# Optimization experiments

Hardware: AMD Instinct MI355X
Metric: run time of the kernel (lower is better)

## Reference

```python
import jax, jax.numpy as jnp
import numpy as np

N, H, F, E, K = 4096, 512, 2048, 8, 2  # tokens, hidden, ffn(=4H), experts, top_k


def setup_inputs() -> dict:
    key = jax.random.key(0)
    ks = jax.random.split(key, 7)
    def w(k, shape, fan_in):
        return jax.random.normal(k, shape, dtype=jnp.float32) * (fan_in ** -0.5)
    return {
        "x": jax.random.normal(ks[0], (N, H), dtype=jnp.float32),
        "W_in": w(ks[1], (H, H), H),          # input_proj.weight  [out,in]
        "W_router": w(ks[2], (E, H), H),      # router.gate.weight [E,H]
        "W_gate": w(ks[3], (E, F, H), H),     # per-expert gate_proj.weight
        "W_up": w(ks[4], (E, F, H), H),       # per-expert up_proj.weight
        "W_down": w(ks[5], (E, H, F), F),     # per-expert down_proj.weight
        "W_out": w(ks[6], (H, H), H),         # output_proj.weight
    }


def reference(x, W_in, W_router, W_gate, W_up, W_down, W_out):
    h = x @ W_in.T                                  # [N,H] input_proj
    logits = h @ W_router.T                         # [N,E]
    # route_mode='balanced' and world_size==1 -> expert_bias is None
    probs = jax.nn.softmax(logits, axis=-1)
    top_w, top_i = jax.lax.top_k(probs, K)          # [N,K]
    top_w = jax.nn.softmax(top_w, axis=-1)          # renormalize over top-k

    # per-token combine weight for each expert: [N,E]
    onehot = jax.nn.one_hot(top_i, E, dtype=h.dtype)      # [N,K,E]
    combine_w = jnp.einsum('nk,nke->ne', top_w, onehot)

    def expert(wg, wu, wd):
        # SwiGLU FFN: down( silu(gate(h)) * up(h) )
        return (jax.nn.silu(h @ wg.T) * (h @ wu.T)) @ wd.T  # [N,H]

    expert_out = jax.vmap(expert)(W_gate, W_up, W_down)     # [E,N,H]
    combined = jnp.einsum('ne,enh->nh', combine_w, expert_out)
    return combined @ W_out.T                                # output_proj
```

## Files before the change

kernel.cpp:

```cpp
#include <hip/hip_runtime.h>
#include <hip/hip_bf16.h>

typedef unsigned short u16;
typedef unsigned int u32;
typedef short bf16x8 __attribute__((ext_vector_type(8)));
typedef float f32x4 __attribute__((ext_vector_type(4)));

#define AS1 __attribute__((address_space(1)))
#define AS3 __attribute__((address_space(3)))

#define NTOK 4096
#define HDIM 512
#define FDIM 2048
#define NEXP 8
#define NASSIGN (NTOK * 2)
#define NPAD2 (NASSIGN + NEXP * 256)
#define RBMAX 128

__device__ __forceinline__ void g2l16(const void* g, void* l) {
  __builtin_amdgcn_global_load_lds((const AS1 u32*)g, (AS3 u32*)l, 16, 0, 0);
}
__device__ __forceinline__ u16 f2bf(float f) {
  u32 u = __float_as_uint(f);
  u = (u + 0x7FFFu + ((u >> 16) & 1u)) >> 16;
  return (u16)u;
}
__device__ __forceinline__ float bf2f(u16 h) { return __uint_as_float(((u32)h) << 16); }
__device__ __forceinline__ u32 pkbf(float a, float b) {
  __hip_bfloat162 h = __float22bfloat162_rn(float2{a, b});
  u32 r;
  __builtin_memcpy(&r, &h, 4);
  return r;
}
__device__ __forceinline__ int4 pk8(const float4 a, const float4 b) {
  int4 r;
  r.x = (int)pkbf(a.x, a.y); r.y = (int)pkbf(a.z, a.w);
  r.z = (int)pkbf(b.x, b.y); r.w = (int)pkbf(b.z, b.w);
  return r;
}

#define WAITV4() asm volatile("s_waitcnt vmcnt(4)" ::: "memory")
#define WAITV0() asm volatile("s_waitcnt vmcnt(0)" ::: "memory")
#define LGKM0() asm volatile("s_waitcnt lgkmcnt(0)" ::: "memory")
#define BAR() __builtin_amdgcn_s_barrier()
#define SCB() __builtin_amdgcn_sched_barrier(0)
#define PRIO1() __builtin_amdgcn_s_setprio(1)
#define PRIO0() __builtin_amdgcn_s_setprio(0)
#define VMBAR() do { WAITV0(); BAR(); } while (0)

__global__ __launch_bounds__(256) void cvtall_kernel(
    const float* __restrict__ x, const float* __restrict__ Wi, const float* __restrict__ Wo,
    const float* __restrict__ Wg, const float* __restrict__ Wu, const float* __restrict__ Wd,
    u16* __restrict__ xb, u16* __restrict__ Wib, u16* __restrict__ Wob,
    u16* __restrict__ Wgb, u16* __restrict__ Wub, u16* __restrict__ Wdb) {
  const int c = blockIdx.x, tid = threadIdx.x;
  const float* s; u16* d; int cs;
  if (c < 128) { s = x; d = xb; cs = 0; }
  else if (c < 144) { s = Wi; d = Wib; cs = 128; }
  else if (c < 160) { s = Wo; d = Wob; cs = 144; }
  else if (c < 672) { s = Wg; d = Wgb; cs = 160; }
  else if (c < 1184) { s = Wu; d = Wub; cs = 672; }
  else { s = Wd; d = Wdb; cs = 1184; }
  const size_t base = (size_t)(c - cs) * 16384 + (size_t)tid * 8;
  const float* sp = s + base;
  u16* dp = d + base;
  float4 a[16];
#pragma unroll
  for (int j = 0; j < 8; ++j) {
    a[2 * j] = *(const float4*)(sp + j * 2048);
    a[2 * j + 1] = *(const float4*)(sp + j * 2048 + 4);
  }
#pragma unroll
  for (int j = 0; j < 8; ++j)
    *(int4*)(dp + j * 2048) = pk8(a[2 * j], a[2 * j + 1]);
}

__global__ __launch_bounds__(256) void wreff_kernel(
    const float* __restrict__ Wr, const float* __restrict__ Wi, double* __restrict__ wre) {
  const int t = blockIdx.x * 256 + threadIdx.x;
  const int e = t >> 9, k = t & 511;
  const float* wr = Wr + e * HDIM;
  double a0 = 0.0, a1 = 0.0, a2 = 0.0, a3 = 0.0;
  for (int j = 0; j < HDIM; j += 4) {
    a0 += (double)wr[j + 0] * (double)Wi[(j + 0) * HDIM + k];
    a1 += (double)wr[j + 1] * (double)Wi[(j + 1) * HDIM + k];
    a2 += (double)wr[j + 2] * (double)Wi[(j + 2) * HDIM + k];
    a3 += (double)wr[j + 3] * (double)Wi[(j + 3) * HDIM + k];
  }
  wre[t] = (a0 + a1) + (a2 + a3);
}

__global__ __launch_bounds__(128) void router_kernel(
    const float* __restrict__ x, const double* __restrict__ wre,
    int* __restrict__ idx, float* __restrict__ wts) {
  __shared__ double lw[NEXP * HDIM];
  for (int i = threadIdx.x; i < NEXP * HDIM; i += 128) lw[i] = wre[i];
  __syncthreads();
  const int n = blockIdx.x * 128 + threadIdx.x;
  const float* xr = x + (size_t)n * HDIM;
  double acc[NEXP] = {};
  for (int k4 = 0; k4 < HDIM / 4; ++k4) {
    const float4 xv = ((const float4*)xr)[k4];
    const float xc[4] = {xv.x, xv.y, xv.z, xv.w};
#pragma unroll
    for (int c = 0; c < 4; ++c) {
      const double xd = (double)xc[c];
#pragma unroll
      for (int e = 0; e < NEXP; ++e) acc[e] += xd * lw[e * HDIM + k4 * 4 + c];
    }
  }
  double mx = acc[0];
#pragma unroll
  for (int e = 1; e < NEXP; ++e) mx = acc[e] > mx ? acc[e] : mx;
  double p[NEXP], se = 0.0;
#pragma unroll
  for (int e = 0; e < NEXP; ++e) { p[e] = exp(acc[e] - mx); se += p[e]; }
  const double inv = 1.0 / se;
#pragma unroll
  for (int e = 0; e < NEXP; ++e) p[e] *= inv;
  int i0 = 0; double b0 = p[0];
#pragma unroll
  for (int e = 1; e < NEXP; ++e) if (p[e] > b0) { b0 = p[e]; i0 = e; }
  int i1 = -1; double b1 = -1.0;
#pragma unroll
  for (int e = 0; e < NEXP; ++e) if (e != i0 && p[e] > b1) { b1 = p[e]; i1 = e; }
  const double e0 = exp(b0), e1 = exp(b1);
  idx[2 * n] = i0; idx[2 * n + 1] = i1;
  wts[2 * n] = (float)(e0 / (e0 + e1));
  wts[2 * n + 1] = (float)(e1 / (e0 + e1));
}

__global__ void assign_kernel(const int* __restrict__ idx, int* __restrict__ tok,
                              int* __restrict__ pos, int* __restrict__ rbe2,
                              int* __restrict__ rbp2, int* __restrict__ rbe1,
                              int* __restrict__ rbp1, int* __restrict__ nrb) {
  __shared__ int cnt[NEXP], cur[NEXP];
  const int tid = threadIdx.x;
  if (tid < NEXP) cnt[tid] = 0;
  __syncthreads();
  for (int a = tid; a < NASSIGN; a += 256) atomicAdd(&cnt[idx[a]], 1);
  __syncthreads();
  if (tid == 0) {
    int o = 0, n2 = 0, n1 = 0;
    for (int e = 0; e < NEXP; ++e) {
      cur[e] = o;
      const int nb2 = (cnt[e] + 255) >> 8;
      const int nb1 = (cnt[e] + 127) >> 7;
      for (int i = 0; i < nb2; ++i) { rbe2[n2] = e; rbp2[n2] = o + i * 256; ++n2; }
      for (int i = 0; i < nb1; ++i) { rbe1[n1] = e; rbp1[n1] = o + i * 128; ++n1; }
      o += nb2 * 256;
    }
    nrb[0] = n2; nrb[1] = n1;
  }
  __syncthreads();
  for (int p = tid; p < NPAD2; p += 256) tok[p] = 0;
  __syncthreads();
  for (int a = tid; a < NASSIGN; a += 256) {
    const int e = idx[a];
    const int q = atomicAdd(&cur[e], 1);
    tok[q] = a >> 1;
    pos[a] = q;
  }
}

template <int SB, int NT>
__device__ __forceinline__ void gemm128_body(
    const u16* __restrict__ A, const u16* __restrict__ B, void* __restrict__ C,
    int m0, int n0, int N, int K, u16* sm, int tid) {
  u16 *lA0 = sm, *lA1 = sm + 8192, *lB0 = sm + 16384, *lB1 = sm + 24576;
  const int w = tid >> 6, l = tid & 63;
  const int wm = (w >> 2) * 64, wn = (w & 3) * 32;
  const int lm = l & 15, lk = (l >> 4) * 8, xr = (l & 7) << 3;
  const int sr = l >> 3, sc = ((l & 7) ^ sr) * 8;
  const u16* As = A + (size_t)(m0 + w * 8 + sr) * K + sc;
  const u16* Bs = B + (size_t)(n0 + w * 8 + sr) * K + sc;
  f32x4 acc[4][2] = {};
  auto STG = [&](u16* dA, u16* dB, int kt) {
    g2l16(As + kt, dA + w * 512);
    g2l16(As + (size_t)64 * K + kt, dA + 4096 + w * 512);
    g2l16(Bs + kt, dB + w * 512);
    g2l16(Bs + (size_t)64 * K + kt, dB + 4096 + w * 512);
  };
  auto CMP = [&](const u16* a_, const u16* b_) {
#pragma unroll
    for (int kk = 0; kk < 2; ++kk) {
      const int ko = (kk * 32 + lk) ^ xr;
      bf16x8 af[4], bf[2];
#pragma unroll
      for (int i = 0; i < 4; ++i) af[i] = *(const bf16x8*)(a_ + (wm + i * 16 + lm) * 64 + ko);
#pragma unroll
      for (int j = 0; j < 2; ++j) bf[j] = *(const bf16x8*)(b_ + (wn + j * 16 + lm) * 64 + ko);
      PRIO1();
#pragma unroll
      for (int i = 0; i < 4; ++i)
#pragma unroll
        for (int j = 0; j < 2; ++j)
          acc[i][j] = __builtin_amdgcn_mfma_f32_16x16x32_bf16(af[i], bf[j], acc[i][j], 0, 0, 0);
      PRIO0();
    }
  };
  STG(lA0, lB0, 0);
  VMBAR();
  for (int t = 0; t < NT; t += 2) {
    if (t + 1 < NT) STG(lA1, lB1, (t + 1) * 64);
    CMP(lA0, lB0);
    VMBAR();
    if (t + 2 < NT) STG(lA0, lB0, (t + 2) * 64);
    CMP(lA1, lB1);
    VMBAR();
  }
  const int cr = (l >> 4) * 4, cc = lm;
#pragma unroll
  for (int i = 0; i < 4; ++i)
#pragma unroll
    for (int j = 0; j < 2; ++j)
#pragma unroll
      for (int r = 0; r < 4; ++r) {
        const size_t o = (size_t)(m0 + wm + i * 16 + cr + r) * N + n0 + wn + j * 16 + cc;
        if (SB) ((u16*)C)[o] = f2bf(acc[i][j][r]);
        else ((float*)C)[o] = acc[i][j][r];
      }
}

__global__ __launch_bounds__(512, 2) void ingemm_kernel(
    const u16* __restrict__ xb, const u16* __restrict__ Wib, u16* __restrict__ hb) {
  __shared__ __align__(16) u16 sm[32768];
  gemm128_body<1, 8>(xb, Wib, hb, blockIdx.y * 128, blockIdx.x * 128, HDIM, HDIM, sm, threadIdx.x);
}

__global__ __launch_bounds__(512, 2) void outgemm_kernel(
    const u16* __restrict__ cb, const u16* __restrict__ Wob, float* __restrict__ out) {
  __shared__ __align__(16) u16 sm[32768];
  gemm128_body<0, 8>(cb, Wob, out, blockIdx.y * 128, blockIdx.x * 128, HDIM, HDIM, sm, threadIdx.x);
}

__global__ __launch_bounds__(512, 2) void gateup_kernel(
    const u16* __restrict__ hb, const u16* __restrict__ Wg, const u16* __restrict__ Wu,
    u16* __restrict__ act, const int* __restrict__ tok, const int* __restrict__ rbe2,
    const int* __restrict__ rbp2, const int* __restrict__ nrb) {
  const int rb = blockIdx.y;
  if (rb >= nrb[0]) return;
  __shared__ __align__(16) u16 sm[65536];
  const int e = rbe2[rb], p0 = rbp2[rb], n0 = blockIdx.x * 128;
  const int tid = threadIdx.x, w = tid >> 6, l = tid & 63;
  const int half = w >> 2, rh = (w >> 1) & 1, ch = w & 1;
  const int lm = l & 15, lk = (l >> 4) * 8, xr = (l & 7) << 3;
  const int sr = l >> 3, sc = ((l & 7) ^ sr) * 8;
  const u16* Asrc[4];
#pragma unroll
  for (int c = 0; c < 4; ++c)
    Asrc[c] = hb + (size_t)tok[p0 + c * 64 + w * 8 + sr] * HDIM + sc;
  const u16 *Gsrc[2], *Usrc[2];
#pragma unroll
  for (int c = 0; c < 2; ++c) {
    Gsrc[c] = Wg + (size_t)e * FDIM * HDIM + (size_t)(n0 + c * 64 + w * 8 + sr) * HDIM + sc;
    Usrc[c] = Wu + (size_t)e * FDIM * HDIM + (size_t)(n0 + c * 64 + w * 8 + sr) * HDIM + sc;
  }
  f32x4 acc[8][4] = {};
  auto STG = [&](int b, int kt) {
    u16* d = sm + b * 32768;
#pragma unroll
    for (int c = 0; c < 4; ++c) g2l16(Asrc[c] + kt, d + c * 4096 + w * 512);
#pragma unroll
    for (int c = 0; c < 2; ++c) {
      g2l16(Gsrc[c] + kt, d + 16384 + c * 4096 + w * 512);
      g2l16(Usrc[c] + kt, d + 24576 + c * 4096 + w * 512);
    }
  };
  auto CMP = [&](int b) {
    const u16* A_ = sm + b * 32768;
    const u16* B_ = A_ + 16384 + half * 8192;
#pragma unroll
    for (int kk = 0; kk < 2; ++kk) {
      const int ko = (kk * 32 + lk) ^ xr;
      bf16x8 af[8], bf[4];
#pragma unroll
      for (int i = 0; i < 8; ++i)
        af[i] = *(const bf16x8*)(A_ + (rh * 128 + i * 16 + lm) * 64 + ko);
#pragma unroll
      for (int j = 0; j < 4; ++j)
        bf[j] = *(const bf16x8*)(B_ + (ch * 64 + j * 16 + lm) * 64 + ko);
      PRIO1();
#pragma unroll
      for (int i = 0; i < 8; ++i)
#pragma unroll
        for (int j = 0; j < 4; ++j)
          acc[i][j] = __builtin_amdgcn_mfma_f32_16x16x32_bf16(af[i], bf[j], acc[i][j], 0, 0, 0);
      PRIO0();
    }
  };
  STG(0, 0);
  VMBAR();
#pragma unroll
  for (int t = 0; t < 8; ++t) {
    if (t < 7) STG((t + 1) & 1, (t + 1) * 64);
    CMP(t & 1);
    VMBAR();
  }
  const int cr = (l >> 4) * 4, cc = lm;
  float* red = (float*)sm;
  if (half == 1) {
#pragma unroll
    for (int i = 0; i < 8; ++i)
#pragma unroll
      for (int j = 0; j < 4; ++j)
        *(f32x4*)&red[(w - 4) * 8192 + (i * 4 + j) * 256 + l * 4] = acc[i][j];
  }
  LGKM0();
  BAR();
  if (half == 0) {
#pragma unroll
    for (int i = 0; i < 8; ++i)
#pragma unroll
      for (int j = 0; j < 4; ++j) {
        const f32x4 ua = *(const f32x4*)&red[w * 8192 + (i * 4 + j) * 256 + l * 4];
#pragma unroll
        for (int r = 0; r < 4; ++r) {
          const float g = acc[i][j][r], u = ua[r];
          const float s = g / (1.0f + __expf(-g));
          act[(size_t)(p0 + rh * 128 + i * 16 + cr + r) * FDIM + n0 + ch * 64 + j * 16 + cc] =
              f2bf(s * u);
        }
      }
  }
}

__global__ __launch_bounds__(512, 2) void down_kernel(
    const u16* __restrict__ act, const u16* __restrict__ Wd, u16* __restrict__ dwn,
    const int* __restrict__ rbe1, const int* __restrict__ rbp1, const int* __restrict__ nrb) {
  const int rb = blockIdx.y;
  if (rb >= nrb[1]) return;
  __shared__ __align__(16) u16 sm[49152];
  const int e = rbe1[rb], p0 = rbp1[rb], n0 = blockIdx.x * 128;
  const int tid = threadIdx.x, w = tid >> 6, l = tid & 63;
  const int g = w >> 2;
  const int wm = ((w >> 1) & 1) * 64, wn = (w & 1) * 64;
  const int lm = l & 15, lk = (l >> 4) * 8, xr = (l & 7) << 3;
  const int ko = (g * 32 + lk) ^ xr;
  const int sr = l >> 3, sc = ((l & 7) ^ sr) * 8;
  const u16* As = act + (size_t)(p0 + w * 8 + sr) * FDIM + sc;
  const u16* Bs = Wd + (size_t)e * HDIM * FDIM + (size_t)(n0 + w * 8 + sr) * FDIM + sc;
  f32x4 acc[4][4] = {};
  auto STG = [&](int b, int kt) {
    u16* d = sm + b * 16384;
    g2l16(As + kt, d + w * 512);
    g2l16(As + (size_t)64 * FDIM + kt, d + 4096 + w * 512);
    g2l16(Bs + kt, d + 8192 + w * 512);
    g2l16(Bs + (size_t)64 * FDIM + kt, d + 12288 + w * 512);
  };
  auto CMP = [&](int b) {
    const u16* a_ = sm + b * 16384;
    const u16* b_ = a_ + 8192;
    bf16x8 af[4], bf[4];
#pragma unroll
    for (int i = 0; i < 4; ++i) af[i] = *(const bf16x8*)(a_ + (wm + i * 16 + lm) * 64 + ko);
#pragma unroll
    for (int j = 0; j < 4; ++j) bf[j] = *(const bf16x8*)(b_ + (wn + j * 16 + lm) * 64 + ko);
#pragma unroll
    for (int i = 0; i < 4; ++i)
#pragma unroll
      for (int j = 0; j < 4; ++j)
        acc[i][j] = __builtin_amdgcn_mfma_f32_16x16x32_bf16(af[i], bf[j], acc[i][j], 0, 0, 0);
  };
  STG(0, 0); STG(1, 64);
  WAITV4(); BAR();
#pragma unroll
  for (int t = 0; t < 32; ++t) {
    if (t + 2 < 32) STG((t + 2) % 3, (t + 2) * 64);
    CMP(t % 3);
    if (t + 2 < 32) WAITV4(); else WAITV0();
    BAR();
  }
  LGKM0();
  SCB();
  BAR();
  float* red = (float*)sm;
  if (g == 1) {
#pragma unroll
    for (int i = 0; i < 4; ++i)
#pragma unroll
      for (int j = 0; j < 4; ++j)
        *(f32x4*)&red[(w & 3) * 4096 + (i * 4 + j) * 256 + l * 4] = acc[i][j];
  }
  BAR();
  if (g == 0) {
    const int cr = (l >> 4) * 4, cc = lm;
#pragma unroll
    for (int i = 0; i < 4; ++i)
#pragma unroll
      for (int j = 0; j < 4; ++j) {
        const f32x4 o = *(const f32x4*)&red[w * 4096 + (i * 4 + j) * 256 + l * 4];
        const f32x4 s = acc[i][j] + o;
#pragma unroll
        for (int r = 0; r < 4; ++r)
          dwn[(size_t)(p0 + wm + i * 16 + cr + r) * HDIM + n0 + wn + j * 16 + cc] = f2bf(s[r]);
      }
  }
}

__global__ void combine_kernel(const u16* __restrict__ dwn, const int* __restrict__ pos,
                               const float* __restrict__ wts, u16* __restrict__ cb) {
  const int n = blockIdx.x, t = threadIdx.x;
  const int p0 = pos[2 * n], p1 = pos[2 * n + 1];
  const float w0 = wts[2 * n], w1 = wts[2 * n + 1];
  const ushort4 a = ((const ushort4*)(dwn + (size_t)p0 * HDIM))[t];
  const ushort4 b = ((const ushort4*)(dwn + (size_t)p1 * HDIM))[t];
  ushort4 o;
  o.x = f2bf(w0 * bf2f(a.x) + w1 * bf2f(b.x));
  o.y = f2bf(w0 * bf2f(a.y) + w1 * bf2f(b.y));
  o.z = f2bf(w0 * bf2f(a.z) + w1 * bf2f(b.z));
  o.w = f2bf(w0 * bf2f(a.w) + w1 * bf2f(b.w));
  ((ushort4*)(cb + (size_t)n * HDIM))[t] = o;
}

extern "C" void kernel_launch(void* const* d_in, const int* in_sizes, int n_in,
                              void* d_out, int out_size, void* d_ws, size_t ws_size,
                              hipStream_t stream) {
  const float* x  = (const float*)d_in[0];
  const float* Wi = (const float*)d_in[1];
  const float* Wr = (const float*)d_in[2];
  const float* Wg = (const float*)d_in[3];
  const float* Wu = (const float*)d_in[4];
  const float* Wd = (const float*)d_in[5];
  const float* Wo = (const float*)d_in[6];
  float* out = (float*)d_out;

  char* ws = (char*)d_ws;
  size_t off = 0;
  auto alloc = [&](size_t bytes) -> void* {
    off = (off + 255) & ~(size_t)255;
    void* p = ws + off;
    off += bytes;
    return p;
  };
  u16* xb   = (u16*)alloc((size_t)NTOK * HDIM * 2);
  u16* hb   = (u16*)alloc((size_t)NTOK * HDIM * 2);
  u16* cb   = (u16*)alloc((size_t)NTOK * HDIM * 2);
  u16* Wib  = (u16*)alloc((size_t)HDIM * HDIM * 2);
  u16* Wob  = (u16*)alloc((size_t)HDIM * HDIM * 2);
  u16* Wgb  = (u16*)alloc((size_t)NEXP * FDIM * HDIM * 2);
  u16* Wub  = (u16*)alloc((size_t)NEXP * FDIM * HDIM * 2);
  u16* Wdb  = (u16*)alloc((size_t)NEXP * HDIM * FDIM * 2);
  u16* actb = (u16*)alloc((size_t)NPAD2 * FDIM * 2);
  u16* dwn  = (u16*)alloc((size_t)NPAD2 * HDIM * 2);
  double* wre = (double*)alloc((size_t)NEXP * HDIM * 8);
  int* idx = (int*)alloc((size_t)NASSIGN * 4);
  float* wts = (float*)alloc((size_t)NASSIGN * 4);
  int* tok = (int*)alloc((size_t)NPAD2 * 4);
  int* pos = (int*)alloc((size_t)NASSIGN * 4);
  int* rbe2 = (int*)alloc((size_t)RBMAX * 4);
  int* rbp2 = (int*)alloc((size_t)RBMAX * 4);
  int* rbe1 = (int*)alloc((size_t)RBMAX * 4);
  int* rbp1 = (int*)alloc((size_t)RBMAX * 4);
  int* nrb = (int*)alloc(256);

  cvtall_kernel<<<1696, 256, 0, stream>>>(x, Wi, Wo, Wg, Wu, Wd, xb, Wib, Wob, Wgb, Wub, Wdb);
  wreff_kernel<<<16, 256, 0, stream>>>(Wr, Wi, wre);
  router_kernel<<<32, 128, 0, stream>>>(x, wre, idx, wts);
  assign_kernel<<<1, 256, 0, stream>>>(idx, tok, pos, rbe2, rbp2, rbe1, rbp1, nrb);
  ingemm_kernel<<<dim3(4, 32), 512, 0, stream>>>(xb, Wib, hb);
  gateup_kernel<<<dim3(16, 40), 512, 0, stream>>>(hb, Wgb, Wub, actb, tok, rbe2, rbp2, nrb);
  down_kernel<<<dim3(4, 72), 512, 0, stream>>>(actb, Wdb, dwn, rbe1, rbp1, nrb);
  combine_kernel<<<NTOK, 128, 0, stream>>>(dwn, pos, wts, cb);
  outgemm_kernel<<<dim3(4, 32), 512, 0, stream>>>(cb, Wob, out);
}
```

Before: 235.2 us.

## Restructure gate/up GEMM main loop into 4-phase interleaved LDS-load/MFMA schedule

```diff
diff --git a/kernel.cpp b/kernel.cpp
--- a/kernel.cpp
+++ b/kernel.cpp
@@ -243,82 +243,117 @@
   __shared__ __align__(16) u16 sm[65536];
   const int e = rbe2[rb], p0 = rbp2[rb], n0 = blockIdx.x * 128;
   const int tid = threadIdx.x, w = tid >> 6, l = tid & 63;
-  const int half = w >> 2, rh = (w >> 1) & 1, ch = w & 1;
+  const int wr = w >> 2, wc = w & 3;
   const int lm = l & 15, lk = (l >> 4) * 8, xr = (l & 7) << 3;
   const int sr = l >> 3, sc = ((l & 7) ^ sr) * 8;
+  const int ko0 = lk ^ xr, ko1 = (32 + lk) ^ xr;
   const u16* Asrc[4];
 #pragma unroll
   for (int c = 0; c < 4; ++c)
     Asrc[c] = hb + (size_t)tok[p0 + c * 64 + w * 8 + sr] * HDIM + sc;
-  const u16 *Gsrc[2], *Usrc[2];
+  const u16 *Gs[2], *Us[2];
 #pragma unroll
   for (int c = 0; c < 2; ++c) {
-    Gsrc[c] = Wg + (size_t)e * FDIM * HDIM + (size_t)(n0 + c * 64 + w * 8 + sr) * HDIM + sc;
-    Usrc[c] = Wu + (size_t)e * FDIM * HDIM + (size_t)(n0 + c * 64 + w * 8 + sr) * HDIM + sc;
+    Gs[c] = Wg + (size_t)e * FDIM * HDIM + (size_t)(n0 + c * 64 + w * 8 + sr) * HDIM + sc;
+    Us[c] = Wu + (size_t)e * FDIM * HDIM + (size_t)(n0 + c * 64 + w * 8 + sr) * HDIM + sc;
   }
   f32x4 acc[8][4] = {};
-  auto STG = [&](int b, int kt) {
-    u16* d = sm + b * 32768;
-#pragma unroll
-    for (int c = 0; c < 4; ++c) g2l16(Asrc[c] + kt, d + c * 4096 + w * 512);
+  auto STGA = [&](int b, int kt) {
+#pragma unroll
+    for (int c = 0; c < 4; ++c) g2l16(Asrc[c] + kt, sm + b * 32768 + c * 4096 + w * 512);
+  };
+  auto STGW = [&](int b, int kt) {
 #pragma unroll
     for (int c = 0; c < 2; ++c) {
-      g2l16(Gsrc[c] + kt, d + 16384 + c * 4096 + w * 512);
-      g2l16(Usrc[c] + kt, d + 24576 + c * 4096 + w * 512);
+      g2l16(Gs[c] + kt, sm + b * 32768 + 16384 + c * 4096 + w * 512);
+      g2l16(Us[c] + kt, sm + b * 32768 + 24576 + c * 4096 + w * 512);
     }
   };
-  auto CMP = [&](int b) {
-    const u16* A_ = sm + b * 32768;
-    const u16* B_ = A_ + 16384 + half * 8192;
-#pragma unroll
-    for (int kk = 0; kk < 2; ++kk) {
-      const int ko = (kk * 32 + lk) ^ xr;
-      bf16x8 af[8], bf[4];
-#pragma unroll
-      for (int i = 0; i < 8; ++i)
-        af[i] = *(const bf16x8*)(A_ + (rh * 128 + i * 16 + lm) * 64 + ko);
-#pragma unroll
-      for (int j = 0; j < 4; ++j)
-        bf[j] = *(const bf16x8*)(B_ + (ch * 64 + j * 16 + lm) * 64 + ko);
-      PRIO1();
-#pragma unroll
-      for (int i = 0; i < 8; ++i)
-#pragma unroll
-        for (int j = 0; j < 4; ++j)
-          acc[i][j] = __builtin_amdgcn_mfma_f32_16x16x32_bf16(af[i], bf[j], acc[i][j], 0, 0, 0);
-      PRIO0();
-    }
-  };
-  STG(0, 0);
-  VMBAR();
-#pragma unroll
+  STGA(0, 0); STGW(0, 0);
+  WAITV0(); BAR();
   for (int t = 0; t < 8; ++t) {
-    if (t < 7) STG((t + 1) & 1, (t + 1) * 64);
-    CMP(t & 1);
-    VMBAR();
+    const u16* A_ = sm + (t & 1) * 32768;
+    const u16* W_ = A_ + 16384;
+    const int nb = (t + 1) & 1;
+    bf16x8 af[4], bf[4];
+#pragma unroll
+    for (int i = 0; i < 4; ++i) af[i] = *(const bf16x8*)(A_ + (wr * 128 + i * 16 + lm) * 64 + ko0);
+#pragma unroll
+    for (int j = 0; j < 4; ++j) bf[j] = *(const bf16x8*)(W_ + (wc * 64 + j * 16 + lm) * 64 + ko0);
+    if (t < 7) STGA(nb, (t + 1) * 64);
+    BAR(); LGKM0(); SCB();
+    PRIO1();
+#pragma unroll
+    for (int i = 0; i < 4; ++i)
+#pragma unroll
+      for (int j = 0; j < 4; ++j)
+        acc[i][j] = __builtin_amdgcn_mfma_f32_16x16x32_bf16(af[i], bf[j], acc[i][j], 0, 0, 0);
+    PRIO0();
+    BAR();
+#pragma unroll
+    for (int i = 0; i < 4; ++i)
+      af[i] = *(const bf16x8*)(A_ + (wr * 128 + (i + 4) * 16 + lm) * 64 + ko0);
+    if (t < 7) STGW(nb, (t + 1) * 64);
+    BAR(); LGKM0(); SCB();
+    PRIO1();
+#pragma unroll
+    for (int i = 0; i < 4; ++i)
+#pragma unroll
+      for (int j = 0; j < 4; ++j)
+        acc[i + 4][j] = __builtin_amdgcn_mfma_f32_16x16x32_bf16(af[i], bf[j], acc[i + 4][j], 0, 0, 0);
+    PRIO0();
+    BAR();
+#pragma unroll
+    for (int i = 0; i < 4; ++i) af[i] = *(const bf16x8*)(A_ + (wr * 128 + i * 16 + lm) * 64 + ko1);
+#pragma unroll
+    for (int j = 0; j < 4; ++j) bf[j] = *(const bf16x8*)(W_ + (wc * 64 + j * 16 + lm) * 64 + ko1);
+    BAR(); LGKM0(); SCB();
+    PRIO1();
+#pragma unroll
+    for (int i = 0; i < 4; ++i)
+#pragma unroll
+      for (int j = 0; j < 4; ++j)
+        acc[i][j] = __builtin_amdgcn_mfma_f32_16x16x32_bf16(af[i], bf[j], acc[i][j], 0, 0, 0);
+    PRIO0();
+    BAR();
+#pragma unroll
+    for (int i = 0; i < 4; ++i)
+      af[i] = *(const bf16x8*)(A_ + (wr * 128 + (i + 4) * 16 + lm) * 64 + ko1);
+    BAR(); LGKM0(); SCB();
+    PRIO1();
+#pragma unroll
+    for (int i = 0; i < 4; ++i)
+#pragma unroll
+      for (int j = 0; j < 4; ++j)
+        acc[i + 4][j] = __builtin_amdgcn_mfma_f32_16x16x32_bf16(af[i], bf[j], acc[i + 4][j], 0, 0, 0);
+    PRIO0();
+    if (t < 7) WAITV0();
+    BAR();
   }
   const int cr = (l >> 4) * 4, cc = lm;
   float* red = (float*)sm;
-  if (half == 1) {
+  if (wc >= 2) {
+    const int uw = wr * 2 + (wc - 2);
 #pragma unroll
     for (int i = 0; i < 8; ++i)
 #pragma unroll
       for (int j = 0; j < 4; ++j)
-        *(f32x4*)&red[(w - 4) * 8192 + (i * 4 + j) * 256 + l * 4] = acc[i][j];
+        *(f32x4*)&red[uw * 8192 + (i * 4 + j) * 256 + l * 4] = acc[i][j];
   }
   LGKM0();
   BAR();
-  if (half == 0) {
+  if (wc < 2) {
+    const int pw = wr * 2 + wc;
 #pragma unroll
     for (int i = 0; i < 8; ++i)
 #pragma unroll
       for (int j = 0; j < 4; ++j) {
-        const f32x4 ua = *(const f32x4*)&red[w * 8192 + (i * 4 + j) * 256 + l * 4];
+        const f32x4 ua = *(const f32x4*)&red[pw * 8192 + (i * 4 + j) * 256 + l * 4];
 #pragma unroll
         for (int r = 0; r < 4; ++r) {
           const float g = acc[i][j][r], u = ua[r];
           const float s = g / (1.0f + __expf(-g));
-          act[(size_t)(p0 + rh * 128 + i * 16 + cr + r) * FDIM + n0 + ch * 64 + j * 16 + cc] =
+          act[(size_t)(p0 + wr * 128 + i * 16 + cr + r) * FDIM + n0 + wc * 64 + j * 16 + cc] =
               f2bf(s * u);
         }
       }
```

Result: slower. 247.5 us (+5.3%).
